# Kernel optimization log

Measured on AMD Instinct MI355X. Metric: run time of the kernel, lower is better.

## Reference

```python
import jax, jax.numpy as jnp
import numpy as np

N = 196608   # total bonds in batch
H = 256      # hidden_size
NH = 8       # num_heads
D = H // NH  # att_size = 32
S = 4096     # num molecules (segments)
EPS = 1e-5


def setup_inputs() -> dict:
    key = jax.random.key(0)
    ks = jax.random.split(key, 12)
    f32 = jnp.float32
    return {
        "message": jax.random.normal(ks[0], (N, H), f32),
        "W_q": jax.random.normal(ks[1], (H, H), f32) * 0.05,
        "W_k": jax.random.normal(ks[2], (H, H), f32) * 0.05,
        "W_v": jax.random.normal(ks[3], (H, H), f32) * 0.05,
        "W_r": jax.random.normal(ks[4], (D, D), f32) * 0.15,
        "w_alpha": jax.random.normal(ks[5], (D,), f32),
        "w_beta": jax.random.normal(ks[6], (D,), f32),
        "W_o": jax.random.normal(ks[7], (H, H), f32) * 0.05,
        "b_o": jax.random.normal(ks[8], (H,), f32) * 0.02,
        "gamma": 1.0 + 0.1 * jax.random.normal(ks[9], (H,), f32),
        "beta_ln": 0.1 * jax.random.normal(ks[10], (H,), f32),
        "segment_ids": jnp.sort(jax.random.randint(ks[11], (N,), 0, S, dtype=jnp.int32)),
        "num_segments": S,
    }


def reference(message, W_q, W_k, W_v, W_r, w_alpha, w_beta, W_o, b_o,
              gamma, beta_ln, segment_ids, num_segments):
    scale = D ** (-0.5)
    # projections (torch Linear: y = x @ W.T), split heads -> [N, NH, D]
    q = (message @ W_q.T).reshape(-1, NH, D)
    k = (message @ W_k.T).reshape(-1, NH, D)
    v = (message @ W_v.T).reshape(-1, NH, D)
    # additive attention: softmax over feature dim d (per bond, per head)
    alpha = jax.nn.softmax(q * w_alpha * scale, axis=-1)
    # global query: sum over bonds within each molecule -> [S, NH, D]
    gq = jax.ops.segment_sum(alpha * q, segment_ids, num_segments=num_segments)
    p = gq[segment_ids] * k                      # [N, NH, D]
    beta = jax.nn.softmax(p * w_beta * scale, axis=-1)
    gk = jax.ops.segment_sum(beta * p, segment_ids, num_segments=num_segments)
    kvi = gk[segment_ids] * v                    # key-value interaction [N, NH, D]
    out = jnp.einsum('nhd,ed->nhe', kvi, W_r) + q  # weight_r on d, residual with q
    out = jax.nn.relu(out)                       # chemprop ReLU activation; dropout p=0
    out = out.reshape(-1, NH * D)
    out = out @ W_o.T + b_o
    # LayerNorm over hidden dim
    mu = jnp.mean(out, axis=-1, keepdims=True)
    var = jnp.mean(jnp.square(out - mu), axis=-1, keepdims=True)
    out = (out - mu) * jax.lax.rsqrt(var + EPS) * gamma + beta_ln
    # prepend cached zero vector (padding row), as the torch loop does for i == 0
    zero = jnp.zeros((1, H), dtype=out.dtype)
    return jnp.concatenate([zero, out], axis=0)
```

## Files before the change

kernel.cpp:

```cpp
#include <hip/hip_runtime.h>
#include <hip/hip_bf16.h>
#include <type_traits>

#define N_BONDS 196608
#define HID     256
#define NSEG    4096
#define SMSCALE 0.17677669529663687f
#define LN_EPS  1e-5f
#define CHUNK   8

typedef __hip_bfloat16 bf16;
typedef __attribute__((ext_vector_type(8))) short short8_t;
typedef __attribute__((ext_vector_type(4))) float f32x4_t;

__device__ __forceinline__ float bf2f(bf16 x) { return __bfloat162float(x); }
__device__ __forceinline__ short f2bs(float f) {
    union { bf16 b; short s; } cv; cv.b = __float2bfloat16(f); return cv.s;
}
__device__ __forceinline__ float us2f(ushort u) {
    union { ushort u; bf16 b; } cv; cv.u = u; return __bfloat162float(cv.b);
}

__device__ __forceinline__ float gsum32(float x) {
#pragma unroll
    for (int m = 16; m >= 1; m >>= 1) x += __shfl_xor(x, m);
    return x;
}

__global__ void cast_kernel(const float* __restrict__ src, ushort* __restrict__ dst, int n4) {
    int i = blockIdx.x * blockDim.x + threadIdx.x;
    const int stride = gridDim.x * blockDim.x;
    for (; i < n4; i += stride) {
        float4 v = reinterpret_cast<const float4*>(src)[i];
        union { ushort4 u; bf16 b[4]; } cv;
        cv.b[0] = __float2bfloat16(v.x);
        cv.b[1] = __float2bfloat16(v.y);
        cv.b[2] = __float2bfloat16(v.z);
        cv.b[3] = __float2bfloat16(v.w);
        reinterpret_cast<ushort4*>(dst)[i] = cv.u;
    }
}

template <typename AT, typename OutT>
__global__ __launch_bounds__(256, 2) void gemm_bt(const AT* __restrict__ A,
                                                  const float* __restrict__ W,
                                                  OutT* __restrict__ C) {
    __shared__ __align__(16) char lds[128 * 512];
    const int t = threadIdx.x;
    const int colhalf = blockIdx.y;
#pragma unroll
    for (int it = 0; it < 16; ++it) {
        int c = it * 256 + t;
        int j = c >> 5, kc = c & 31;
        const float* wp = W + ((colhalf << 7) + j) * HID + (kc << 3);
        float4 w0 = *reinterpret_cast<const float4*>(wp);
        float4 w1 = *reinterpret_cast<const float4*>(wp + 4);
        union { uint4 u; short s[8]; } cv;
        cv.s[0] = f2bs(w0.x); cv.s[1] = f2bs(w0.y); cv.s[2] = f2bs(w0.z); cv.s[3] = f2bs(w0.w);
        cv.s[4] = f2bs(w1.x); cv.s[5] = f2bs(w1.y); cv.s[6] = f2bs(w1.z); cv.s[7] = f2bs(w1.w);
        *reinterpret_cast<uint4*>(lds + j * 512 + ((kc << 4) ^ ((j & 7) << 4))) = cv.u;
    }
    __syncthreads();

    const int wave = t >> 6, lane = t & 63;
    const int lr = lane & 15, lk = lane >> 4;
    const long rowbase = (long)blockIdx.x * 128 + wave * 32;

    f32x4_t acc[2][8];
#pragma unroll
    for (int r = 0; r < 2; ++r)
#pragma unroll
        for (int cc = 0; cc < 8; ++cc) acc[r][cc] = (f32x4_t){0.f, 0.f, 0.f, 0.f};

    const AT* a0 = A + (rowbase + lr) * HID;
    const AT* a1 = a0 + 16 * HID;
#pragma unroll
    for (int k0 = 0; k0 < HID; k0 += 32) {
        const int koff = k0 + lk * 8;
        short8_t af0, af1;
        if constexpr (std::is_same_v<AT, float>) {
            float4 x0 = *reinterpret_cast<const float4*>(a0 + koff);
            float4 x1 = *reinterpret_cast<const float4*>(a0 + koff + 4);
            float4 y0 = *reinterpret_cast<const float4*>(a1 + koff);
            float4 y1 = *reinterpret_cast<const float4*>(a1 + koff + 4);
            af0[0] = f2bs(x0.x); af0[1] = f2bs(x0.y); af0[2] = f2bs(x0.z); af0[3] = f2bs(x0.w);
            af0[4] = f2bs(x1.x); af0[5] = f2bs(x1.y); af0[6] = f2bs(x1.z); af0[7] = f2bs(x1.w);
            af1[0] = f2bs(y0.x); af1[1] = f2bs(y0.y); af1[2] = f2bs(y0.z); af1[3] = f2bs(y0.w);
            af1[4] = f2bs(y1.x); af1[5] = f2bs(y1.y); af1[6] = f2bs(y1.z); af1[7] = f2bs(y1.w);
        } else {
            af0 = *reinterpret_cast<const short8_t*>(a0 + koff);
            af1 = *reinterpret_cast<const short8_t*>(a1 + koff);
        }
#pragma unroll
        for (int cc = 0; cc < 8; ++cc) {
            const int j = cc * 16 + lr;
            short8_t bfr = *reinterpret_cast<const short8_t*>(
                lds + j * 512 + (((k0 << 1) + (lk << 4)) ^ ((j & 7) << 4)));
            acc[0][cc] = __builtin_amdgcn_mfma_f32_16x16x32_bf16(af0, bfr, acc[0][cc], 0, 0, 0);
            acc[1][cc] = __builtin_amdgcn_mfma_f32_16x16x32_bf16(af1, bfr, acc[1][cc], 0, 0, 0);
        }
    }
#pragma unroll
    for (int r = 0; r < 2; ++r) {
#pragma unroll
        for (int cc = 0; cc < 8; ++cc) {
            const int col = (colhalf << 7) + cc * 16 + lr;
#pragma unroll
            for (int reg = 0; reg < 4; ++reg) {
                const long row = rowbase + r * 16 + lk * 4 + reg;
                const float v = acc[r][cc][reg];
                if constexpr (sizeof(OutT) == 2) C[row * HID + col] = __float2bfloat16(v);
                else                             C[row * HID + col] = v;
            }
        }
    }
}

__global__ __launch_bounds__(256, 2) void qkv_gemm(const ushort* __restrict__ A,
                                                   const float* __restrict__ Wq,
                                                   const float* __restrict__ Wk,
                                                   const float* __restrict__ Wv,
                                                   bf16* __restrict__ Q,
                                                   bf16* __restrict__ K,
                                                   bf16* __restrict__ V) {
    __shared__ __align__(16) char lds[128 * 512];
    const int t = threadIdx.x;
    const int which = blockIdx.y >> 1;
    const int colhalf = blockIdx.y & 1;
    const float* W = (which == 0) ? Wq : (which == 1) ? Wk : Wv;
    bf16* C = (which == 0) ? Q : (which == 1) ? K : V;

#pragma unroll
    for (int it = 0; it < 16; ++it) {
        int c = it * 256 + t;
        int j = c >> 5, kc = c & 31;
        const float* wp = W + ((colhalf << 7) + j) * HID + (kc << 3);
        float4 w0 = *reinterpret_cast<const float4*>(wp);
        float4 w1 = *reinterpret_cast<const float4*>(wp + 4);
        union { uint4 u; short s[8]; } cv;
        cv.s[0] = f2bs(w0.x); cv.s[1] = f2bs(w0.y); cv.s[2] = f2bs(w0.z); cv.s[3] = f2bs(w0.w);
        cv.s[4] = f2bs(w1.x); cv.s[5] = f2bs(w1.y); cv.s[6] = f2bs(w1.z); cv.s[7] = f2bs(w1.w);
        *reinterpret_cast<uint4*>(lds + j * 512 + ((kc << 4) ^ ((j & 7) << 4))) = cv.u;
    }
    __syncthreads();

    const int wave = t >> 6, lane = t & 63;
    const int lr = lane & 15, lk = lane >> 4;
    const long rowbase = (long)blockIdx.x * 128 + wave * 32;

    f32x4_t acc[2][8];
#pragma unroll
    for (int r = 0; r < 2; ++r)
#pragma unroll
        for (int cc = 0; cc < 8; ++cc) acc[r][cc] = (f32x4_t){0.f, 0.f, 0.f, 0.f};

    const ushort* a0 = A + (rowbase + lr) * HID;
    const ushort* a1 = a0 + 16 * HID;
#pragma unroll
    for (int k0 = 0; k0 < HID; k0 += 32) {
        const int koff = k0 + lk * 8;
        short8_t af0 = *reinterpret_cast<const short8_t*>(a0 + koff);
        short8_t af1 = *reinterpret_cast<const short8_t*>(a1 + koff);
#pragma unroll
        for (int cc = 0; cc < 8; ++cc) {
            const int j = cc * 16 + lr;
            short8_t bfr = *reinterpret_cast<const short8_t*>(
                lds + j * 512 + (((k0 << 1) + (lk << 4)) ^ ((j & 7) << 4)));
            acc[0][cc] = __builtin_amdgcn_mfma_f32_16x16x32_bf16(af0, bfr, acc[0][cc], 0, 0, 0);
            acc[1][cc] = __builtin_amdgcn_mfma_f32_16x16x32_bf16(af1, bfr, acc[1][cc], 0, 0, 0);
        }
    }
#pragma unroll
    for (int r = 0; r < 2; ++r) {
#pragma unroll
        for (int cc = 0; cc < 8; ++cc) {
            const int col = (colhalf << 7) + cc * 16 + lr;
#pragma unroll
            for (int reg = 0; reg < 4; ++reg) {
                const long row = rowbase + r * 16 + lk * 4 + reg;
                C[row * HID + col] = __float2bfloat16(acc[r][cc][reg]);
            }
        }
    }
}

__global__ __launch_bounds__(256) void alpha_gq_kernel(const bf16* __restrict__ qb,
                                                       const float* __restrict__ w_alpha,
                                                       const int* __restrict__ seg,
                                                       float* __restrict__ gq) {
    const int j = threadIdx.x;
    const float wa = w_alpha[j & 31] * SMSCALE;
    const long n0 = (long)blockIdx.x * CHUNK;
    float acc = 0.f;
    int cur = -1;
    for (int i = 0; i < CHUNK; ++i) {
        const long n = n0 + i;
        const int s = seg[n];
        const float qv = bf2f(qb[n * HID + j]);
        const float e = __expf(qv * wa);
        const float ssum = gsum32(e);
        const float alpha = e / ssum;
        if (s != cur) {
            if (cur >= 0) atomicAdd(&gq[(long)cur * HID + j], acc);
            acc = 0.f;
            cur = s;
        }
        acc += alpha * qv;
    }
    atomicAdd(&gq[(long)cur * HID + j], acc);
}

__global__ __launch_bounds__(256) void beta_gk_kernel(const bf16* __restrict__ kb,
                                                      const float* __restrict__ gq,
                                                      const float* __restrict__ w_beta,
                                                      const int* __restrict__ seg,
                                                      float* __restrict__ gk) {
    const int j = threadIdx.x;
    const float wb = w_beta[j & 31] * SMSCALE;
    const long n0 = (long)blockIdx.x * CHUNK;
    float acc = 0.f;
    int cur = -1;
    for (int i = 0; i < CHUNK; ++i) {
        const long n = n0 + i;
        const int s = seg[n];
        const float kv = bf2f(kb[n * HID + j]);
        const float p = gq[(long)s * HID + j] * kv;
        const float e = __expf(p * wb);
        const float ssum = gsum32(e);
        const float beta = e / ssum;
        if (s != cur) {
            if (cur >= 0) atomicAdd(&gk[(long)cur * HID + j], acc);
            acc = 0.f;
            cur = s;
        }
        acc += beta * p;
    }
    atomicAdd(&gk[(long)cur * HID + j], acc);
}

__global__ __launch_bounds__(256) void act_mfma_kernel(const ushort* __restrict__ vb,
                                                       const ushort* __restrict__ qb,
                                                       const float* __restrict__ gk,
                                                       const float* __restrict__ Wr,
                                                       const int* __restrict__ seg,
                                                       ushort* __restrict__ act) {
    const int t = threadIdx.x;
    const int wave = t >> 6, lane = t & 63;
    const int lr = lane & 15, lk = lane >> 4;

    short8_t bhi[2], blo[2];
#pragma unroll
    for (int ct = 0; ct < 2; ++ct) {
        const float* wr = Wr + (ct * 16 + lr) * 32 + lk * 8;
#pragma unroll
        for (int e = 0; e < 8; ++e) {
            const float w = wr[e];
            const short h = f2bs(w);
            bhi[ct][e] = h;
            blo[ct][e] = f2bs(w - us2f((ushort)h));
        }
    }

    const long rowblock = (long)blockIdx.x * 256 + wave * 64;
#pragma unroll
    for (int rt = 0; rt < 4; ++rt) {
        const long rtbase = rowblock + rt * 16;
        const long arow = rtbase + lr;
        const int n = (int)(arow >> 3), h = (int)(arow & 7);
        const int sid = seg[n];
        short8_t v8 = *reinterpret_cast<const short8_t*>(vb + arow * 32 + lk * 8);
        const float* gp = gk + (long)sid * HID + h * 32 + lk * 8;
        float4 g0 = *reinterpret_cast<const float4*>(gp);
        float4 g1 = *reinterpret_cast<const float4*>(gp + 4);
        float kvi[8];
        kvi[0] = g0.x * us2f((ushort)v8[0]);
        kvi[1] = g0.y * us2f((ushort)v8[1]);
        kvi[2] = g0.z * us2f((ushort)v8[2]);
        kvi[3] = g0.w * us2f((ushort)v8[3]);
        kvi[4] = g1.x * us2f((ushort)v8[4]);
        kvi[5] = g1.y * us2f((ushort)v8[5]);
        kvi[6] = g1.z * us2f((ushort)v8[6]);
        kvi[7] = g1.w * us2f((ushort)v8[7]);
        short8_t ahi, alo;
#pragma unroll
        for (int e = 0; e < 8; ++e) {
            const short hh = f2bs(kvi[e]);
            ahi[e] = hh;
            alo[e] = f2bs(kvi[e] - us2f((ushort)hh));
        }
#pragma unroll
        for (int ct = 0; ct < 2; ++ct) {
            f32x4_t c = (f32x4_t){0.f, 0.f, 0.f, 0.f};
            c = __builtin_amdgcn_mfma_f32_16x16x32_bf16(ahi, bhi[ct], c, 0, 0, 0);
            c = __builtin_amdgcn_mfma_f32_16x16x32_bf16(alo, bhi[ct], c, 0, 0, 0);
            c = __builtin_amdgcn_mfma_f32_16x16x32_bf16(ahi, blo[ct], c, 0, 0, 0);
#pragma unroll
            for (int reg = 0; reg < 4; ++reg) {
                const long row = rtbase + lk * 4 + reg;
                const long idx = row * 32 + ct * 16 + lr;
                act[idx] = (ushort)f2bs(fmaxf(c[reg] + us2f(qb[idx]), 0.f));
            }
        }
    }
}

__global__ __launch_bounds__(256) void ln_kernel(const ushort* __restrict__ tmp,
                                                 const float* __restrict__ b_o,
                                                 const float* __restrict__ gamma,
                                                 const float* __restrict__ beta_ln,
                                                 float* __restrict__ out) {
    const int wave = threadIdx.x >> 6, lane = threadIdx.x & 63;
    const long row = (long)blockIdx.x * 4 + wave;
    const float4 bo = reinterpret_cast<const float4*>(b_o)[lane];
    const float4 g = reinterpret_cast<const float4*>(gamma)[lane];
    const float4 bl = reinterpret_cast<const float4*>(beta_ln)[lane];
    const ushort4 xr = reinterpret_cast<const ushort4*>(tmp + row * HID)[lane];
    float4 x = {us2f(xr.x) + bo.x, us2f(xr.y) + bo.y, us2f(xr.z) + bo.z, us2f(xr.w) + bo.w};
    float s = x.x + x.y + x.z + x.w;
#pragma unroll
    for (int m = 32; m >= 1; m >>= 1) s += __shfl_xor(s, m);
    const float mu = s * (1.f / HID);
    float4 dx = {x.x - mu, x.y - mu, x.z - mu, x.w - mu};
    float sq = dx.x * dx.x + dx.y * dx.y + dx.z * dx.z + dx.w * dx.w;
#pragma unroll
    for (int m = 32; m >= 1; m >>= 1) sq += __shfl_xor(sq, m);
    const float r = rsqrtf(sq * (1.f / HID) + LN_EPS);
    float4 o;
    o.x = dx.x * r * g.x + bl.x;
    o.y = dx.y * r * g.y + bl.y;
    o.z = dx.z * r * g.z + bl.z;
    o.w = dx.w * r * g.w + bl.w;
    reinterpret_cast<float4*>(out + (row + 1) * HID)[lane] = o;
}

extern "C" void kernel_launch(void* const* d_in, const int* in_sizes, int n_in,
                              void* d_out, int out_size, void* d_ws, size_t ws_size,
                              hipStream_t stream) {
    const float* msg    = (const float*)d_in[0];
    const float* Wq     = (const float*)d_in[1];
    const float* Wk     = (const float*)d_in[2];
    const float* Wv     = (const float*)d_in[3];
    const float* Wr     = (const float*)d_in[4];
    const float* walpha = (const float*)d_in[5];
    const float* wbeta  = (const float*)d_in[6];
    const float* Wo     = (const float*)d_in[7];
    const float* bo     = (const float*)d_in[8];
    const float* gamma  = (const float*)d_in[9];
    const float* betaln = (const float*)d_in[10];
    const int*   seg    = (const int*)d_in[11];

    char* ws = (char*)d_ws;
    const size_t nh = (size_t)N_BONDS * HID;
    size_t off = 0;
    bf16* msgb = (bf16*)(ws + off); off += nh * 2;
    bf16* qb   = (bf16*)(ws + off); off += nh * 2;
    bf16* kb   = (bf16*)(ws + off); off += nh * 2;
    bf16* vb   = (bf16*)(ws + off); off += nh * 2;
    float* gq  = (float*)(ws + off); off += (size_t)NSEG * HID * 4;
    float* gk  = (float*)(ws + off); off += (size_t)NSEG * HID * 4;
    bf16*  act = msgb;
    bf16*  tmp = qb;

    hipMemsetAsync(gq, 0, (size_t)2 * NSEG * HID * 4, stream);
    hipMemsetAsync(d_out, 0, HID * sizeof(float), stream);

    cast_kernel<<<4096, 256, 0, stream>>>(msg, (ushort*)msgb, (int)(nh / 4));

    dim3 gqkv(N_BONDS / 128, 6);
    qkv_gemm<<<gqkv, 256, 0, stream>>>((const ushort*)msgb, Wq, Wk, Wv, qb, kb, vb);

    alpha_gq_kernel<<<N_BONDS / CHUNK, 256, 0, stream>>>(qb, walpha, seg, gq);
    beta_gk_kernel<<<N_BONDS / CHUNK, 256, 0, stream>>>(kb, gq, wbeta, seg, gk);

    act_mfma_kernel<<<N_BONDS * 8 / 256, 256, 0, stream>>>((const ushort*)vb, (const ushort*)qb,
                                                           gk, Wr, seg, (ushort*)act);

    dim3 gg(N_BONDS / 128, 2);
    gemm_bt<ushort, bf16><<<gg, 256, 0, stream>>>((const ushort*)act, Wo, tmp);
    ln_kernel<<<N_BONDS / 4, 256, 0, stream>>>((const ushort*)tmp, bo, gamma, betaln, (float*)d_out);
}
```

Measured before the change: 590.1 us.

## Stage activation tile in LDS once and loop over Q/K/V weights in QKV GEMM

The QKV GEMM now stages each 128-row tile of the bf16 message into LDS once and computes all three projections and both column halves inside one block, reading bf16 weights straight from global memory. Previously six blocks per row tile each re-read the activations and re-converted fp32 weights into LDS. Weights are pre-cast to bf16 by three small extra cast launches. This cuts activation traffic and removes redundant weight conversion, at the cost of a sixfold smaller grid, fewer blocks to hide latency, and weight fragments loaded uncoalesced from L2/global instead of LDS.

```diff
diff --git a/kernel.cpp b/kernel.cpp
--- a/kernel.cpp
+++ b/kernel.cpp
@@ -117,68 +117,67 @@
 }
 
 __global__ __launch_bounds__(256, 2) void qkv_gemm(const ushort* __restrict__ A,
-                                                   const float* __restrict__ Wq,
-                                                   const float* __restrict__ Wk,
-                                                   const float* __restrict__ Wv,
+                                                   const ushort* __restrict__ Wqb,
+                                                   const ushort* __restrict__ Wkb,
+                                                   const ushort* __restrict__ Wvb,
                                                    bf16* __restrict__ Q,
                                                    bf16* __restrict__ K,
                                                    bf16* __restrict__ V) {
     __shared__ __align__(16) char lds[128 * 512];
     const int t = threadIdx.x;
-    const int which = blockIdx.y >> 1;
-    const int colhalf = blockIdx.y & 1;
-    const float* W = (which == 0) ? Wq : (which == 1) ? Wk : Wv;
-    bf16* C = (which == 0) ? Q : (which == 1) ? K : V;
+    const long row0 = (long)blockIdx.x * 128;
 
 #pragma unroll
     for (int it = 0; it < 16; ++it) {
         int c = it * 256 + t;
         int j = c >> 5, kc = c & 31;
-        const float* wp = W + ((colhalf << 7) + j) * HID + (kc << 3);
-        float4 w0 = *reinterpret_cast<const float4*>(wp);
-        float4 w1 = *reinterpret_cast<const float4*>(wp + 4);
-        union { uint4 u; short s[8]; } cv;
-        cv.s[0] = f2bs(w0.x); cv.s[1] = f2bs(w0.y); cv.s[2] = f2bs(w0.z); cv.s[3] = f2bs(w0.w);
-        cv.s[4] = f2bs(w1.x); cv.s[5] = f2bs(w1.y); cv.s[6] = f2bs(w1.z); cv.s[7] = f2bs(w1.w);
-        *reinterpret_cast<uint4*>(lds + j * 512 + ((kc << 4) ^ ((j & 7) << 4))) = cv.u;
+        uint4 val = *reinterpret_cast<const uint4*>(A + (row0 + j) * HID + (kc << 3));
+        *reinterpret_cast<uint4*>(lds + j * 512 + ((kc << 4) ^ ((j & 7) << 4))) = val;
     }
     __syncthreads();
 
     const int wave = t >> 6, lane = t & 63;
     const int lr = lane & 15, lk = lane >> 4;
-    const long rowbase = (long)blockIdx.x * 128 + wave * 32;
-
-    f32x4_t acc[2][8];
-#pragma unroll
-    for (int r = 0; r < 2; ++r)
-#pragma unroll
-        for (int cc = 0; cc < 8; ++cc) acc[r][cc] = (f32x4_t){0.f, 0.f, 0.f, 0.f};
-
-    const ushort* a0 = A + (rowbase + lr) * HID;
-    const ushort* a1 = a0 + 16 * HID;
-#pragma unroll
-    for (int k0 = 0; k0 < HID; k0 += 32) {
-        const int koff = k0 + lk * 8;
-        short8_t af0 = *reinterpret_cast<const short8_t*>(a0 + koff);
-        short8_t af1 = *reinterpret_cast<const short8_t*>(a1 + koff);
-#pragma unroll
-        for (int cc = 0; cc < 8; ++cc) {
-            const int j = cc * 16 + lr;
-            short8_t bfr = *reinterpret_cast<const short8_t*>(
-                lds + j * 512 + (((k0 << 1) + (lk << 4)) ^ ((j & 7) << 4)));
-            acc[0][cc] = __builtin_amdgcn_mfma_f32_16x16x32_bf16(af0, bfr, acc[0][cc], 0, 0, 0);
-            acc[1][cc] = __builtin_amdgcn_mfma_f32_16x16x32_bf16(af1, bfr, acc[1][cc], 0, 0, 0);
-        }
-    }
-#pragma unroll
-    for (int r = 0; r < 2; ++r) {
-#pragma unroll
-        for (int cc = 0; cc < 8; ++cc) {
-            const int col = (colhalf << 7) + cc * 16 + lr;
-#pragma unroll
-            for (int reg = 0; reg < 4; ++reg) {
-                const long row = rowbase + r * 16 + lk * 4 + reg;
-                C[row * HID + col] = __float2bfloat16(acc[r][cc][reg]);
+    const int r0 = wave * 32 + lr;
+    const int r1 = r0 + 16;
+
+#pragma unroll
+    for (int m = 0; m < 3; ++m) {
+        const ushort* W = (m == 0) ? Wqb : (m == 1) ? Wkb : Wvb;
+        bf16* C = (m == 0) ? Q : (m == 1) ? K : V;
+#pragma unroll
+        for (int ch = 0; ch < 2; ++ch) {
+            f32x4_t acc[2][8];
+#pragma unroll
+            for (int r = 0; r < 2; ++r)
+#pragma unroll
+                for (int cc = 0; cc < 8; ++cc) acc[r][cc] = (f32x4_t){0.f, 0.f, 0.f, 0.f};
+
+#pragma unroll
+            for (int k0 = 0; k0 < HID; k0 += 32) {
+                short8_t af0 = *reinterpret_cast<const short8_t*>(
+                    lds + r0 * 512 + (((k0 << 1) + (lk << 4)) ^ ((lr & 7) << 4)));
+                short8_t af1 = *reinterpret_cast<const short8_t*>(
+                    lds + r1 * 512 + (((k0 << 1) + (lk << 4)) ^ ((lr & 7) << 4)));
+#pragma unroll
+                for (int cc = 0; cc < 8; ++cc) {
+                    const int j = (ch << 7) + cc * 16 + lr;
+                    short8_t bfr = *reinterpret_cast<const short8_t*>(W + j * HID + k0 + lk * 8);
+                    acc[0][cc] = __builtin_amdgcn_mfma_f32_16x16x32_bf16(af0, bfr, acc[0][cc], 0, 0, 0);
+                    acc[1][cc] = __builtin_amdgcn_mfma_f32_16x16x32_bf16(af1, bfr, acc[1][cc], 0, 0, 0);
+                }
+            }
+#pragma unroll
+            for (int r = 0; r < 2; ++r) {
+#pragma unroll
+                for (int cc = 0; cc < 8; ++cc) {
+                    const int col = (ch << 7) + cc * 16 + lr;
+#pragma unroll
+                    for (int reg = 0; reg < 4; ++reg) {
+                        const long row = row0 + wave * 32 + r * 16 + lk * 4 + reg;
+                        C[row * HID + col] = __float2bfloat16(acc[r][cc][reg]);
+                    }
+                }
             }
         }
     }
@@ -358,6 +357,9 @@
     bf16* vb   = (bf16*)(ws + off); off += nh * 2;
     float* gq  = (float*)(ws + off); off += (size_t)NSEG * HID * 4;
     float* gk  = (float*)(ws + off); off += (size_t)NSEG * HID * 4;
+    bf16* wqb  = (bf16*)(ws + off); off += (size_t)HID * HID * 2;
+    bf16* wkb  = (bf16*)(ws + off); off += (size_t)HID * HID * 2;
+    bf16* wvb  = (bf16*)(ws + off); off += (size_t)HID * HID * 2;
     bf16*  act = msgb;
     bf16*  tmp = qb;
 
@@ -365,9 +367,13 @@
     hipMemsetAsync(d_out, 0, HID * sizeof(float), stream);
 
     cast_kernel<<<4096, 256, 0, stream>>>(msg, (ushort*)msgb, (int)(nh / 4));
-
-    dim3 gqkv(N_BONDS / 128, 6);
-    qkv_gemm<<<gqkv, 256, 0, stream>>>((const ushort*)msgb, Wq, Wk, Wv, qb, kb, vb);
+    cast_kernel<<<32, 256, 0, stream>>>(Wq, (ushort*)wqb, HID * HID / 4);
+    cast_kernel<<<32, 256, 0, stream>>>(Wk, (ushort*)wkb, HID * HID / 4);
+    cast_kernel<<<32, 256, 0, stream>>>(Wv, (ushort*)wvb, HID * HID / 4);
+
+    qkv_gemm<<<N_BONDS / 128, 256, 0, stream>>>((const ushort*)msgb,
+                                                (const ushort*)wqb, (const ushort*)wkb,
+                                                (const ushort*)wvb, qb, kb, vb);
 
     alpha_gq_kernel<<<N_BONDS / CHUNK, 256, 0, stream>>>(qb, walpha, seg, gq);
     beta_gk_kernel<<<N_BONDS / CHUNK, 256, 0, stream>>>(kb, gq, wbeta, seg, gk);
```

Measured after the change: 733.1 us. +24.2%, slower.
